# Kernel optimization log

Measured on AMD Instinct MI355X. Metric: run time of the kernel, lower is better.

## Reference

```python
import jax, jax.numpy as jnp
import numpy as np

B, S, D, H = 1, 2048, 4096, 32
HD = D // H              # 128
FF = 11008               # multiple_of rounding of int(2*(4*D)/3)
EPS = 1e-6

def rmsnorm(x, w):
    xf = x.astype(jnp.float32)
    y = xf * jax.lax.rsqrt(jnp.mean(xf * xf, axis=-1, keepdims=True) + EPS)
    return y.astype(x.dtype) * w

def apply_rope(x, cos, sin):
    # x: (B,S,H,HD); complex pairs are adjacent elements (torch view_as_complex)
    xr, xi = x[..., 0::2], x[..., 1::2]
    c = cos[None, :, None, :]
    s = sin[None, :, None, :]
    out_r = xr * c - xi * s
    out_i = xr * s + xi * c
    return jnp.stack([out_r, out_i], axis=-1).reshape(x.shape)

def setup_inputs() -> dict:
    key = jax.random.key(0)
    ks = jax.random.split(key, 9)
    sc = 0.02
    x = jax.random.normal(ks[0], (B, S, D), jnp.float32)
    wq = jax.random.normal(ks[1], (D, D), jnp.float32) * sc
    wk = jax.random.normal(ks[2], (D, D), jnp.float32) * sc
    wv = jax.random.normal(ks[3], (D, D), jnp.float32) * sc
    wo = jax.random.normal(ks[4], (D, D), jnp.float32) * sc
    w1 = jax.random.normal(ks[5], (D, FF), jnp.float32) * sc
    w2 = jax.random.normal(ks[6], (FF, D), jnp.float32) * sc
    w3 = jax.random.normal(ks[7], (D, FF), jnp.float32) * sc
    attn_norm_w = jnp.ones((D,), jnp.float32)
    ffn_norm_w = jnp.ones((D,), jnp.float32)
    # rotary tables (seqlen, head_dim//2), theta=10000 as in LLaMA
    inv_freq = 1.0 / (10000.0 ** (jnp.arange(0, HD, 2, dtype=jnp.float32) / HD))
    t = jnp.arange(S, dtype=jnp.float32)
    freqs = jnp.outer(t, inv_freq)           # (S, HD//2)
    cos, sin = jnp.cos(freqs), jnp.sin(freqs)
    # causal additive mask (1,1,S,S)
    mask = jnp.triu(jnp.full((S, S), -jnp.inf, jnp.float32), k=1)[None, None]
    return {"x": x, "wq": wq, "wk": wk, "wv": wv, "wo": wo,
            "w1": w1, "w2": w2, "w3": w3,
            "attn_norm_w": attn_norm_w, "ffn_norm_w": ffn_norm_w,
            "cos": cos, "sin": sin, "mask": mask}

def reference(x, wq, wk, wv, wo, w1, w2, w3, attn_norm_w, ffn_norm_w, cos, sin, mask):
    # attention sub-block
    hn = rmsnorm(x, attn_norm_w)
    q = (hn @ wq).reshape(B, S, H, HD)
    k = (hn @ wk).reshape(B, S, H, HD)
    v = (hn @ wv).reshape(B, S, H, HD)
    q = apply_rope(q, cos, sin)
    k = apply_rope(k, cos, sin)
    scores = jnp.einsum('bqhd,bkhd->bhqk', q, k) / jnp.sqrt(jnp.float32(HD))
    scores = scores + mask
    p = jax.nn.softmax(scores.astype(jnp.float32), axis=-1).astype(q.dtype)
    attn = jnp.einsum('bhqk,bkhd->bqhd', p, v).reshape(B, S, D) @ wo
    h = x + attn
    # SwiGLU FFN sub-block
    fn = rmsnorm(h, ffn_norm_w)
    ff = (jax.nn.silu(fn @ w1) * (fn @ w3)) @ w2
    return h + ff
```

## Files before the change

kernel.cpp:

```cpp
#include <hip/hip_runtime.h>

#define S_LEN 2048
#define DIM   4096
#define NH    32
#define HD    128
#define FF    11008

#define BM 128
#define BN 128
#define BK 32

typedef __attribute__((ext_vector_type(8))) short bf16x8;
typedef __attribute__((ext_vector_type(4))) float f32x4;

enum { GF_OUTF32 = 1, GF_CSKIP = 2, GF_CKLIM = 4, GF_RES = 8 };

__device__ __forceinline__ unsigned short f2b(float f) {
  union { float f; unsigned int u; } v; v.f = f;
  return (unsigned short)((v.u + 0x7FFFu + ((v.u >> 16) & 1u)) >> 16);
}
__device__ __forceinline__ float b2f(unsigned short b) {
  union { unsigned int u; float f; } v; v.u = ((unsigned int)b) << 16;
  return v.f;
}

__device__ __forceinline__ void gload16(const unsigned short* g, unsigned short* l) {
  __builtin_amdgcn_global_load_lds(
      (const __attribute__((address_space(1))) void*)g,
      (__attribute__((address_space(3))) void*)l,
      16, 0, 0);
}

__global__ __launch_bounds__(256) void gemm_bt(
    const unsigned short* __restrict__ A, int lda, long bsA,
    const unsigned short* __restrict__ Bt, int ldb, long bsB,
    void* __restrict__ Cv, int ldc, long bsC,
    const float* __restrict__ R,
    int M, int N, int K, float scale, int flags)
{
  const int m0 = blockIdx.y * BM;
  const int n0 = blockIdx.x * BN;
  if ((flags & GF_CSKIP) && n0 > m0 + (BM - 1)) return;
  const int bz = blockIdx.z;
  A  += (long)bz * bsA;
  Bt += (long)bz * bsB;
  int Keff = K;
  if (flags & GF_CKLIM) { int kl = m0 + BM; Keff = kl < K ? kl : K; }

  __shared__ unsigned short As[BM * BK];
  __shared__ unsigned short Bs[BN * BK];

  const int tid  = threadIdx.x;
  const int wave = tid >> 6;
  const int lane = tid & 63;
  const int qd   = lane >> 4;
  const int r16  = lane & 15;
  const int wm   = (wave & 1) * 64;
  const int wn   = (wave >> 1) * 64;

  const int c0 = tid;
  const int mA0 = c0 >> 2, kA0 = (c0 & 3) * 8;
  const int c1 = tid + 256;
  const int mA1 = c1 >> 2, kA1 = (c1 & 3) * 8;
  unsigned short* AsL0 = &As[wave * 512];
  unsigned short* AsL1 = &As[2048 + wave * 512];
  unsigned short* BsL0 = &Bs[wave * 512];
  unsigned short* BsL1 = &Bs[2048 + wave * 512];
  const unsigned short* Abase0 = A  + (long)(m0 + mA0) * lda + kA0;
  const unsigned short* Abase1 = A  + (long)(m0 + mA1) * lda + kA1;
  const unsigned short* Bbase0 = Bt + (long)(n0 + mA0) * ldb + kA0;
  const unsigned short* Bbase1 = Bt + (long)(n0 + mA1) * ldb + kA1;

  f32x4 acc[4][4];
#pragma unroll
  for (int i = 0; i < 4; i++)
#pragma unroll
    for (int j = 0; j < 4; j++)
      acc[i][j] = (f32x4){0.0f, 0.0f, 0.0f, 0.0f};

  for (int k0 = 0; k0 < Keff; k0 += BK) {
    gload16(Abase0 + k0, AsL0);
    gload16(Abase1 + k0, AsL1);
    gload16(Bbase0 + k0, BsL0);
    gload16(Bbase1 + k0, BsL1);
    __syncthreads();
    bf16x8 af[4], bfr[4];
#pragma unroll
    for (int i = 0; i < 4; i++)
      af[i] = *(const bf16x8*)(&As[(wm + i * 16 + r16) * BK + qd * 8]);
#pragma unroll
    for (int j = 0; j < 4; j++)
      bfr[j] = *(const bf16x8*)(&Bs[(wn + j * 16 + r16) * BK + qd * 8]);
#pragma unroll
    for (int i = 0; i < 4; i++)
#pragma unroll
      for (int j = 0; j < 4; j++)
        acc[i][j] = __builtin_amdgcn_mfma_f32_16x16x32_bf16(af[i], bfr[j], acc[i][j], 0, 0, 0);
    __syncthreads();
  }

  float* Cf = (float*)Cv + (long)bz * bsC;
  unsigned short* Ch = (unsigned short*)Cv + (long)bz * bsC;
#pragma unroll
  for (int i = 0; i < 4; i++) {
    const int row = m0 + wm + i * 16 + qd * 4;
#pragma unroll
    for (int j = 0; j < 4; j++) {
      const int col = n0 + wn + j * 16 + r16;
#pragma unroll
      for (int t = 0; t < 4; t++) {
        long idx = (long)(row + t) * ldc + col;
        float v = acc[i][j][t] * scale;
        if (flags & GF_RES) v += R[idx];
        if (flags & GF_OUTF32) Cf[idx] = v;
        else Ch[idx] = f2b(v);
      }
    }
  }
}

__global__ __launch_bounds__(256) void rmsnorm_kernel(const float* __restrict__ x,
                                                      const float* __restrict__ w,
                                                      unsigned short* __restrict__ out)
{
  const long row = blockIdx.x;
  const float* xr = x + row * DIM;
  float vals[16];
  float ss = 0.0f;
#pragma unroll
  for (int t = 0; t < 16; t++) {
    float v = xr[threadIdx.x + t * 256];
    vals[t] = v; ss += v * v;
  }
#pragma unroll
  for (int o = 32; o > 0; o >>= 1) ss += __shfl_down(ss, o, 64);
  __shared__ float red[4];
  const int wv = threadIdx.x >> 6, ln = threadIdx.x & 63;
  if (ln == 0) red[wv] = ss;
  __syncthreads();
  ss = red[0] + red[1] + red[2] + red[3];
  const float scale = 1.0f / sqrtf(ss * (1.0f / (float)DIM) + 1e-6f);
#pragma unroll
  for (int t = 0; t < 16; t++) {
    int c = threadIdx.x + t * 256;
    out[row * DIM + c] = f2b(vals[t] * scale * w[c]);
  }
}

__global__ __launch_bounds__(256) void rope_kernel(unsigned short* __restrict__ xq,
                                                   const float* __restrict__ cosb,
                                                   const float* __restrict__ sinb)
{
  const int idx = blockIdx.x * 256 + threadIdx.x;
  if (idx >= S_LEN * NH * 64) return;
  const int i = idx & 63;
  const int h = (idx >> 6) & (NH - 1);
  const int s = idx >> 11;
  const long base = (long)s * DIM + h * HD + 2 * i;
  const float xr = b2f(xq[base]), xi = b2f(xq[base + 1]);
  const float c = cosb[s * 64 + i], sn = sinb[s * 64 + i];
  xq[base]     = f2b(xr * c - xi * sn);
  xq[base + 1] = f2b(xr * sn + xi * c);
}

__global__ __launch_bounds__(256) void softmax_kernel(unsigned short* __restrict__ sc)
{
  const int s  = blockIdx.x;
  const int hz = blockIdx.y;
  unsigned short* row = sc + ((long)hz * S_LEN + s) * S_LEN;
  __shared__ float buf[S_LEN];
  __shared__ float redA[4], redB[4];
  const int tid = threadIdx.x;
  const int wv = tid >> 6, ln = tid & 63;
  const int valid = s + 1;

  float mx = -3.0e38f;
  for (int c = tid; c < valid; c += 256) { float v = b2f(row[c]); buf[c] = v; mx = fmaxf(mx, v); }
#pragma unroll
  for (int o = 32; o > 0; o >>= 1) mx = fmaxf(mx, __shfl_down(mx, o, 64));
  if (ln == 0) redA[wv] = mx;
  __syncthreads();
  mx = fmaxf(fmaxf(redA[0], redA[1]), fmaxf(redA[2], redA[3]));

  float sum = 0.0f;
  for (int c = tid; c < valid; c += 256) { float e = __expf(buf[c] - mx); buf[c] = e; sum += e; }
#pragma unroll
  for (int o = 32; o > 0; o >>= 1) sum += __shfl_down(sum, o, 64);
  if (ln == 0) redB[wv] = sum;
  __syncthreads();
  sum = redB[0] + redB[1] + redB[2] + redB[3];
  const float inv = 1.0f / sum;
  for (int c = tid; c < S_LEN; c += 256)
    row[c] = (c < valid) ? f2b(buf[c] * inv) : (unsigned short)0;
}

__global__ __launch_bounds__(256) void silu_mul_kernel(const unsigned short* __restrict__ a1,
                                                       const unsigned short* __restrict__ a3,
                                                       unsigned short* __restrict__ o, long n)
{
  const long i = (long)blockIdx.x * 256 + threadIdx.x;
  if (i >= n) return;
  const float xv = b2f(a1[i]);
  const float g = xv / (1.0f + __expf(-xv));
  o[i] = f2b(g * b2f(a3[i]));
}

__global__ __launch_bounds__(256) void transpose_cast_kernel(const float* __restrict__ in,
                                                             unsigned short* __restrict__ out,
                                                             int rows, int cols)
{
  __shared__ unsigned short tile[32][33];
  const int c0 = blockIdx.x * 32, r0 = blockIdx.y * 32;
  const int tx = threadIdx.x & 31, ty = threadIdx.x >> 5;
#pragma unroll
  for (int i = 0; i < 4; i++) {
    int rr = ty + i * 8;
    tile[rr][tx] = f2b(in[(long)(r0 + rr) * cols + (c0 + tx)]);
  }
  __syncthreads();
#pragma unroll
  for (int i = 0; i < 4; i++) {
    int rr = ty + i * 8;
    out[(long)(c0 + rr) * rows + (r0 + tx)] = tile[tx][rr];
  }
}

__global__ __launch_bounds__(256) void transpose_bf16_kernel(const unsigned short* __restrict__ in,
                                                             long in_bs, int ld_in,
                                                             unsigned short* __restrict__ out,
                                                             long out_bs, int ld_out,
                                                             int rows, int cols)
{
  const int b = blockIdx.z;
  in  += (long)b * in_bs;
  out += (long)b * out_bs;
  __shared__ unsigned short tile[32][33];
  const int c0 = blockIdx.x * 32, r0 = blockIdx.y * 32;
  const int tx = threadIdx.x & 31, ty = threadIdx.x >> 5;
#pragma unroll
  for (int i = 0; i < 4; i++)
    tile[ty + i * 8][tx] = in[(long)(r0 + ty + i * 8) * ld_in + (c0 + tx)];
  __syncthreads();
#pragma unroll
  for (int i = 0; i < 4; i++)
    out[(long)(c0 + ty + i * 8) * ld_out + (r0 + tx)] = tile[tx][ty + i * 8];
}

extern "C" void kernel_launch(void* const* d_in, const int* in_sizes, int n_in,
                              void* d_out, int out_size, void* d_ws, size_t ws_size,
                              hipStream_t stream)
{
  const float* x    = (const float*)d_in[0];
  const float* wq   = (const float*)d_in[1];
  const float* wk   = (const float*)d_in[2];
  const float* wv   = (const float*)d_in[3];
  const float* wo   = (const float*)d_in[4];
  const float* w1   = (const float*)d_in[5];
  const float* w2   = (const float*)d_in[6];
  const float* w3   = (const float*)d_in[7];
  const float* anw  = (const float*)d_in[8];
  const float* fnw  = (const float*)d_in[9];
  const float* cosb = (const float*)d_in[10];
  const float* sinb = (const float*)d_in[11];
  float* out = (float*)d_out;

  char* ws = (char*)d_ws;
  size_t o = 0;
  unsigned short* wT   = (unsigned short*)(ws + o); o += 90177536ULL;
  unsigned short* hn   = (unsigned short*)(ws + o); o += 16777216ULL;
  unsigned short* attnb= (unsigned short*)(ws + o); o += 16777216ULL;
  float*          hbuf = (float*)(ws + o);          o += 33554432ULL;
  unsigned short* fn   = (unsigned short*)(ws + o); o += 16777216ULL;
  char* ovl = ws + o;
  unsigned short* qb = (unsigned short*)(ovl);
  unsigned short* kb = (unsigned short*)(ovl + 16777216ULL);
  unsigned short* vb = (unsigned short*)(ovl + 2 * 16777216ULL);
  unsigned short* vT = (unsigned short*)(ovl + 3 * 16777216ULL);
  unsigned short* sc = (unsigned short*)(ovl + 4 * 16777216ULL);
  unsigned short* a1   = (unsigned short*)(ovl);
  unsigned short* a3   = (unsigned short*)(ovl + 45088768ULL);
  unsigned short* ffin = (unsigned short*)(ovl + 2 * 45088768ULL);

  const dim3 blk(256);
  const dim3 tgD(DIM / 32, DIM / 32);
  const dim3 gqkv(DIM / BN, S_LEN / BM, 1);

  rmsnorm_kernel<<<S_LEN, blk, 0, stream>>>(x, anw, hn);

  transpose_cast_kernel<<<tgD, blk, 0, stream>>>(wq, wT, DIM, DIM);
  gemm_bt<<<gqkv, blk, 0, stream>>>(hn, DIM, 0, wT, DIM, 0, qb, DIM, 0, nullptr,
                                    S_LEN, DIM, DIM, 1.0f, 0);
  transpose_cast_kernel<<<tgD, blk, 0, stream>>>(wk, wT, DIM, DIM);
  gemm_bt<<<gqkv, blk, 0, stream>>>(hn, DIM, 0, wT, DIM, 0, kb, DIM, 0, nullptr,
                                    S_LEN, DIM, DIM, 1.0f, 0);
  transpose_cast_kernel<<<tgD, blk, 0, stream>>>(wv, wT, DIM, DIM);
  gemm_bt<<<gqkv, blk, 0, stream>>>(hn, DIM, 0, wT, DIM, 0, vb, DIM, 0, nullptr,
                                    S_LEN, DIM, DIM, 1.0f, 0);

  rope_kernel<<<(S_LEN * NH * 64) / 256, blk, 0, stream>>>(qb, cosb, sinb);
  rope_kernel<<<(S_LEN * NH * 64) / 256, blk, 0, stream>>>(kb, cosb, sinb);

  const dim3 tv(HD / 32, S_LEN / 32, NH);
  transpose_bf16_kernel<<<tv, blk, 0, stream>>>(vb, (long)HD, DIM,
                                                vT, (long)HD * S_LEN, S_LEN, S_LEN, HD);

  const float sscale = 0.08838834764831845f;
  for (int ch = 0; ch < 4; ch++) {
    const int h0 = ch * 8;
    const dim3 gs(S_LEN / BN, S_LEN / BM, 8);
    gemm_bt<<<gs, blk, 0, stream>>>(qb + h0 * HD, DIM, (long)HD,
                                    kb + h0 * HD, DIM, (long)HD,
                                    sc, S_LEN, (long)S_LEN * S_LEN, nullptr,
                                    S_LEN, S_LEN, HD, sscale, GF_CSKIP);
    const dim3 gsm(S_LEN, 8);
    softmax_kernel<<<gsm, blk, 0, stream>>>(sc);
    const dim3 gpv(HD / BN, S_LEN / BM, 8);
    gemm_bt<<<gpv, blk, 0, stream>>>(sc, S_LEN, (long)S_LEN * S_LEN,
                                     vT + (long)h0 * HD * S_LEN, S_LEN, (long)HD * S_LEN,
                                     attnb + h0 * HD, DIM, (long)HD, nullptr,
                                     S_LEN, HD, S_LEN, 1.0f, GF_CKLIM);
  }

  transpose_cast_kernel<<<tgD, blk, 0, stream>>>(wo, wT, DIM, DIM);
  gemm_bt<<<gqkv, blk, 0, stream>>>(attnb, DIM, 0, wT, DIM, 0, hbuf, DIM, 0, x,
                                    S_LEN, DIM, DIM, 1.0f, GF_OUTF32 | GF_RES);

  rmsnorm_kernel<<<S_LEN, blk, 0, stream>>>(hbuf, fnw, fn);

  const dim3 tg1(FF / 32, DIM / 32);
  const dim3 gff(FF / BN, S_LEN / BM, 1);
  transpose_cast_kernel<<<tg1, blk, 0, stream>>>(w1, wT, DIM, FF);
  gemm_bt<<<gff, blk, 0, stream>>>(fn, DIM, 0, wT, DIM, 0, a1, FF, 0, nullptr,
                                   S_LEN, FF, DIM, 1.0f, 0);
  transpose_cast_kernel<<<tg1, blk, 0, stream>>>(w3, wT, DIM, FF);
  gemm_bt<<<gff, blk, 0, stream>>>(fn, DIM, 0, wT, DIM, 0, a3, FF, 0, nullptr,
                                   S_LEN, FF, DIM, 1.0f, 0);

  silu_mul_kernel<<<(S_LEN * FF) / 256, blk, 0, stream>>>(a1, a3, ffin, (long)S_LEN * FF);

  const dim3 tg2(DIM / 32, FF / 32);
  const dim3 gout(DIM / BN, S_LEN / BM, 1);
  transpose_cast_kernel<<<tg2, blk, 0, stream>>>(w2, wT, FF, DIM);
  gemm_bt<<<gout, blk, 0, stream>>>(ffin, FF, 0, wT, FF, 0, out, DIM, 0, hbuf,
                                    S_LEN, DIM, FF, 1.0f, GF_OUTF32 | GF_RES);
}
```

Measured before the change: 2.640 ms.

## Add 256x256 pipelined MFMA GEMM kernel for projection and FFN matmuls

Adds a new GEMM kernel with 256x256x64 tiles and 512 threads, replacing the 128x128 kernel for the Q/K/V/O projections and the three FFN matmuls. It double-buffers LDS and stages global-to-LDS loads in quarter pieces interleaved between MFMA groups, with barriers and wave priority raises. It also remaps block indices so neighbouring tiles land on the same XCD. The aim is more data reuse per tile and better overlap of memory with compute, at the cost of 128KB of LDS per block and heavy register use, which may limit occupancy.

After: 2.478 ms. 1.07x faster.

```diff
diff --git a/kernel.cpp b/kernel.cpp
--- a/kernel.cpp
+++ b/kernel.cpp
@@ -10,6 +10,10 @@
 #define BN 128
 #define BK 32
 
+#define QBM 256
+#define QBN 256
+#define QBK 64
+
 typedef __attribute__((ext_vector_type(8))) short bf16x8;
 typedef __attribute__((ext_vector_type(4))) float f32x4;
 
@@ -29,6 +33,175 @@
       (const __attribute__((address_space(1))) void*)g,
       (__attribute__((address_space(3))) void*)l,
       16, 0, 0);
+}
+
+__global__ __launch_bounds__(512, 2) void gemm256(
+    const unsigned short* __restrict__ A, int lda,
+    const unsigned short* __restrict__ Bt, int ldb,
+    void* __restrict__ Cv, int ldc,
+    const float* __restrict__ R,
+    int M, int N, int K, float scale, int flags)
+{
+  __shared__ unsigned short lds[65536];
+
+  const int nx = gridDim.x;
+  const int nwg = nx * gridDim.y;
+  const int orig = blockIdx.y * nx + blockIdx.x;
+  const int xcd = orig & 7, loc = orig >> 3;
+  const int q8 = nwg >> 3, r8 = nwg & 7;
+  const int swz = (xcd < r8 ? xcd * (q8 + 1) : r8 * (q8 + 1) + (xcd - r8) * q8) + loc;
+  const int m0 = (swz / nx) * QBM;
+  const int n0 = (swz % nx) * QBN;
+
+  const int tid  = threadIdx.x;
+  const int wave = tid >> 6;
+  const int lane = tid & 63;
+  const int qd   = lane >> 4;
+  const int r16  = lane & 15;
+  const int wm   = (wave >> 2) * 128;
+  const int wn   = (wave & 3) * 64;
+
+  const int nt = K / QBK;
+
+  const int srow = tid >> 3;
+  const int sslot = tid & 7;
+
+  auto stage_half = [&](const unsigned short* gRow0, int ld, int ldsBase) {
+    {
+      const int r = srow;
+      gload16(gRow0 + (long)r * ld + ((sslot ^ (r & 7)) << 3),
+              &lds[ldsBase + wave * 512]);
+    }
+    {
+      const int r = srow + 64;
+      gload16(gRow0 + (long)r * ld + ((sslot ^ (r & 7)) << 3),
+              &lds[ldsBase + 4096 + wave * 512]);
+    }
+  };
+  auto stage = [&](int tau, int region) {
+    const int tc = tau < nt ? tau : nt - 1;
+    const int kk = tc * QBK;
+    const int bb = (tau & 1) * 32768;
+    switch (region) {
+      case 0: stage_half(A  + (long)m0         * lda + kk, lda, bb);         break;
+      case 1: stage_half(A  + (long)(m0 + 128) * lda + kk, lda, bb + 8192);  break;
+      case 2: stage_half(Bt + (long)n0         * ldb + kk, ldb, bb + 16384); break;
+      case 3: stage_half(Bt + (long)(n0 + 128) * ldb + kk, ldb, bb + 24576); break;
+    }
+  };
+
+  stage(0, 0); stage(0, 1); stage(0, 2); stage(0, 3);
+  stage(1, 0); stage(1, 1); stage(1, 2);
+  asm volatile("s_waitcnt vmcnt(6)" ::: "memory");
+  asm volatile("s_barrier" ::: "memory");
+
+  f32x4 acc[8][4];
+#pragma unroll
+  for (int i = 0; i < 8; i++)
+#pragma unroll
+    for (int j = 0; j < 4; j++)
+      acc[i][j] = (f32x4){0.0f, 0.0f, 0.0f, 0.0f};
+
+  bf16x8 af[8][2], bf[4][2];
+
+  for (int t = 0; t < nt; ++t) {
+    const int cb = (t & 1) * 32768;
+    const unsigned short* As = &lds[cb];
+    const unsigned short* Bs = &lds[cb + 16384];
+
+#pragma unroll
+    for (int i = 0; i < 8; i++) {
+      const int r = wm + i * 16 + r16;
+#pragma unroll
+      for (int kh = 0; kh < 2; kh++)
+        af[i][kh] = *(const bf16x8*)&As[r * 64 + ((((kh << 2) | qd) ^ (r & 7)) << 3)];
+    }
+#pragma unroll
+    for (int j = 0; j < 2; j++) {
+      const int r = wn + j * 16 + r16;
+#pragma unroll
+      for (int kh = 0; kh < 2; kh++)
+        bf[j][kh] = *(const bf16x8*)&Bs[r * 64 + ((((kh << 2) | qd) ^ (r & 7)) << 3)];
+    }
+    stage(t + 1, 3);
+    asm volatile("s_barrier" ::: "memory");
+    __builtin_amdgcn_s_setprio(1);
+#pragma unroll
+    for (int i = 0; i < 4; i++)
+#pragma unroll
+      for (int j = 0; j < 2; j++)
+#pragma unroll
+        for (int kh = 0; kh < 2; kh++)
+          acc[i][j] = __builtin_amdgcn_mfma_f32_16x16x32_bf16(af[i][kh], bf[j][kh], acc[i][j], 0, 0, 0);
+    __builtin_amdgcn_s_setprio(0);
+    asm volatile("s_barrier" ::: "memory");
+
+#pragma unroll
+    for (int j = 2; j < 4; j++) {
+      const int r = wn + j * 16 + r16;
+#pragma unroll
+      for (int kh = 0; kh < 2; kh++)
+        bf[j][kh] = *(const bf16x8*)&Bs[r * 64 + ((((kh << 2) | qd) ^ (r & 7)) << 3)];
+    }
+    stage(t + 2, 0);
+    asm volatile("s_barrier" ::: "memory");
+    __builtin_amdgcn_s_setprio(1);
+#pragma unroll
+    for (int i = 0; i < 4; i++)
+#pragma unroll
+      for (int j = 2; j < 4; j++)
+#pragma unroll
+        for (int kh = 0; kh < 2; kh++)
+          acc[i][j] = __builtin_amdgcn_mfma_f32_16x16x32_bf16(af[i][kh], bf[j][kh], acc[i][j], 0, 0, 0);
+    __builtin_amdgcn_s_setprio(0);
+    asm volatile("s_barrier" ::: "memory");
+
+    stage(t + 2, 1);
+    asm volatile("s_barrier" ::: "memory");
+    __builtin_amdgcn_s_setprio(1);
+#pragma unroll
+    for (int i = 4; i < 8; i++)
+#pragma unroll
+      for (int j = 2; j < 4; j++)
+#pragma unroll
+        for (int kh = 0; kh < 2; kh++)
+          acc[i][j] = __builtin_amdgcn_mfma_f32_16x16x32_bf16(af[i][kh], bf[j][kh], acc[i][j], 0, 0, 0);
+    __builtin_amdgcn_s_setprio(0);
+    asm volatile("s_barrier" ::: "memory");
+
+    stage(t + 2, 2);
+    asm volatile("s_barrier" ::: "memory");
+    __builtin_amdgcn_s_setprio(1);
+#pragma unroll
+    for (int i = 4; i < 8; i++)
+#pragma unroll
+      for (int j = 0; j < 2; j++)
+#pragma unroll
+        for (int kh = 0; kh < 2; kh++)
+          acc[i][j] = __builtin_amdgcn_mfma_f32_16x16x32_bf16(af[i][kh], bf[j][kh], acc[i][j], 0, 0, 0);
+    __builtin_amdgcn_s_setprio(0);
+    asm volatile("s_waitcnt vmcnt(6)" ::: "memory");
+    asm volatile("s_barrier" ::: "memory");
+  }
+
+  float* Cf = (float*)Cv;
+  unsigned short* Ch = (unsigned short*)Cv;
+#pragma unroll
+  for (int i = 0; i < 8; i++) {
+    const int row = m0 + wm + i * 16 + qd * 4;
+#pragma unroll
+    for (int j = 0; j < 4; j++) {
+      const int col = n0 + wn + j * 16 + r16;
+#pragma unroll
+      for (int tt = 0; tt < 4; tt++) {
+        long idx = (long)(row + tt) * ldc + col;
+        float v = acc[i][j][tt] * scale;
+        if (flags & GF_RES) v += R[idx];
+        if (flags & GF_OUTF32) Cf[idx] = v;
+        else Ch[idx] = f2b(v);
+      }
+    }
+  }
 }
 
 __global__ __launch_bounds__(256) void gemm_bt(
@@ -282,20 +455,22 @@
   unsigned short* ffin = (unsigned short*)(ovl + 2 * 45088768ULL);
 
   const dim3 blk(256);
+  const dim3 blk512(512);
   const dim3 tgD(DIM / 32, DIM / 32);
-  const dim3 gqkv(DIM / BN, S_LEN / BM, 1);
+  const dim3 gD256(DIM / QBN, S_LEN / QBM);
+  const dim3 gFF256(FF / QBN, S_LEN / QBM);
 
   rmsnorm_kernel<<<S_LEN, blk, 0, stream>>>(x, anw, hn);
 
   transpose_cast_kernel<<<tgD, blk, 0, stream>>>(wq, wT, DIM, DIM);
-  gemm_bt<<<gqkv, blk, 0, stream>>>(hn, DIM, 0, wT, DIM, 0, qb, DIM, 0, nullptr,
-                                    S_LEN, DIM, DIM, 1.0f, 0);
+  gemm256<<<gD256, blk512, 0, stream>>>(hn, DIM, wT, DIM, qb, DIM, nullptr,
+                                        S_LEN, DIM, DIM, 1.0f, 0);
   transpose_cast_kernel<<<tgD, blk, 0, stream>>>(wk, wT, DIM, DIM);
-  gemm_bt<<<gqkv, blk, 0, stream>>>(hn, DIM, 0, wT, DIM, 0, kb, DIM, 0, nullptr,
-                                    S_LEN, DIM, DIM, 1.0f, 0);
+  gemm256<<<gD256, blk512, 0, stream>>>(hn, DIM, wT, DIM, kb, DIM, nullptr,
+                                        S_LEN, DIM, DIM, 1.0f, 0);
   transpose_cast_kernel<<<tgD, blk, 0, stream>>>(wv, wT, DIM, DIM);
-  gemm_bt<<<gqkv, blk, 0, stream>>>(hn, DIM, 0, wT, DIM, 0, vb, DIM, 0, nullptr,
-                                    S_LEN, DIM, DIM, 1.0f, 0);
+  gemm256<<<gD256, blk512, 0, stream>>>(hn, DIM, wT, DIM, vb, DIM, nullptr,
+                                        S_LEN, DIM, DIM, 1.0f, 0);
 
   rope_kernel<<<(S_LEN * NH * 64) / 256, blk, 0, stream>>>(qb, cosb, sinb);
   rope_kernel<<<(S_LEN * NH * 64) / 256, blk, 0, stream>>>(kb, cosb, sinb);
@@ -322,25 +497,23 @@
   }
 
   transpose_cast_kernel<<<tgD, blk, 0, stream>>>(wo, wT, DIM, DIM);
-  gemm_bt<<<gqkv, blk, 0, stream>>>(attnb, DIM, 0, wT, DIM, 0, hbuf, DIM, 0, x,
-                                    S_LEN, DIM, DIM, 1.0f, GF_OUTF32 | GF_RES);
+  gemm256<<<gD256, blk512, 0, stream>>>(attnb, DIM, wT, DIM, hbuf, DIM, x,
+                                        S_LEN, DIM, DIM, 1.0f, GF_OUTF32 | GF_RES);
 
   rmsnorm_kernel<<<S_LEN, blk, 0, stream>>>(hbuf, fnw, fn);
 
   const dim3 tg1(FF / 32, DIM / 32);
-  const dim3 gff(FF / BN, S_LEN / BM, 1);
   transpose_cast_kernel<<<tg1, blk, 0, stream>>>(w1, wT, DIM, FF);
-  gemm_bt<<<gff, blk, 0, stream>>>(fn, DIM, 0, wT, DIM, 0, a1, FF, 0, nullptr,
-                                   S_LEN, FF, DIM, 1.0f, 0);
+  gemm256<<<gFF256, blk512, 0, stream>>>(fn, DIM, wT, DIM, a1, FF, nullptr,
+                                         S_LEN, FF, DIM, 1.0f, 0);
   transpose_cast_kernel<<<tg1, blk, 0, stream>>>(w3, wT, DIM, FF);
-  gemm_bt<<<gff, blk, 0, stream>>>(fn, DIM, 0, wT, DIM, 0, a3, FF, 0, nullptr,
-                                   S_LEN, FF, DIM, 1.0f, 0);
+  gemm256<<<gFF256, blk512, 0, stream>>>(fn, DIM, wT, DIM, a3, FF, nullptr,
+                                         S_LEN, FF, DIM, 1.0f, 0);
 
   silu_mul_kernel<<<(S_LEN * FF) / 256, blk, 0, stream>>>(a1, a3, ffin, (long)S_LEN * FF);
 
   const dim3 tg2(DIM / 32, FF / 32);
-  const dim3 gout(DIM / BN, S_LEN / BM, 1);
   transpose_cast_kernel<<<tg2, blk, 0, stream>>>(w2, wT, FF, DIM);
-  gemm_bt<<<gout, blk, 0, stream>>>(ffin, FF, 0, wT, FF, 0, out, DIM, 0, hbuf,
-                                    S_LEN, DIM, FF, 1.0f, GF_OUTF32 | GF_RES);
-}
+  gemm256<<<gD256, blk512, 0, stream>>>(ffin, FF, wT, FF, out, DIM, hbuf,
+                                        S_LEN, DIM, FF, 1.0f, GF_OUTF32 | GF_RES);
+}
```
